# Performance work log

Measured on AMD Instinct MI355X. Metric: run time of the kernel, lower is better.

## Reference

```python
import jax, jax.numpy as jnp
import numpy as np

NUM_SLOTS, SLOT_DIM, INPUT_DIM = 4, 32, 8
NUM_ITERS = 3
SCALE = SLOT_DIM ** -0.5
LN_EPS = 1e-5


def setup_inputs() -> dict:
    key = jax.random.key(0)
    ks = jax.random.split(key, 12)
    B = 65536
    return {
        "latent": jax.random.normal(ks[0], (B, INPUT_DIM, 4, 4), jnp.float32),
        "slot_mu": jax.random.normal(ks[1], (1, NUM_SLOTS, SLOT_DIM), jnp.float32) * 0.1,
        "w_in": jax.random.normal(ks[2], (SLOT_DIM, INPUT_DIM), jnp.float32) * (INPUT_DIM ** -0.5),
        "b_in": jnp.zeros((SLOT_DIM,), jnp.float32),
        "ln_g": jnp.ones((SLOT_DIM,), jnp.float32),
        "ln_b": jnp.zeros((SLOT_DIM,), jnp.float32),
        "wq": jax.random.normal(ks[3], (SLOT_DIM, SLOT_DIM), jnp.float32) * (SLOT_DIM ** -0.5),
        "wk": jax.random.normal(ks[4], (SLOT_DIM, SLOT_DIM), jnp.float32) * (SLOT_DIM ** -0.5),
        "wv": jax.random.normal(ks[5], (SLOT_DIM, SLOT_DIM), jnp.float32) * (SLOT_DIM ** -0.5),
        "gru_wih": jax.random.normal(ks[6], (3 * SLOT_DIM, SLOT_DIM), jnp.float32) * (SLOT_DIM ** -0.5),
        "gru_whh": jax.random.normal(ks[7], (3 * SLOT_DIM, SLOT_DIM), jnp.float32) * (SLOT_DIM ** -0.5),
        "gru_bih": jnp.zeros((3 * SLOT_DIM,), jnp.float32),
        "gru_bhh": jnp.zeros((3 * SLOT_DIM,), jnp.float32),
    }


def _gru_cell(x, h, wih, whh, bih, bbh):
    # torch.nn.GRUCell math. x, h: [M, D]; weights: [3D, D]
    gi = x @ wih.T + bih  # [M, 3D]
    gh = h @ whh.T + bbh
    i_r, i_z, i_n = jnp.split(gi, 3, axis=-1)
    h_r, h_z, h_n = jnp.split(gh, 3, axis=-1)
    r = jax.nn.sigmoid(i_r + h_r)
    z = jax.nn.sigmoid(i_z + h_z)
    n = jnp.tanh(i_n + r * h_n)
    return (1.0 - z) * n + z * h


def reference(latent, slot_mu, w_in, b_in, ln_g, ln_b, wq, wk, wv,
              gru_wih, gru_whh, gru_bih, gru_bhh):
    B, C, H, W = latent.shape
    N = H * W
    x = latent.reshape(B, C, N).transpose(0, 2, 1)  # [B, N, C]
    x = x @ w_in.T + b_in                           # [B, N, D]
    mu = jnp.mean(x, axis=-1, keepdims=True)
    var = jnp.mean(jnp.square(x - mu), axis=-1, keepdims=True)
    x = (x - mu) / jnp.sqrt(var + LN_EPS) * ln_g + ln_b

    slots = jnp.broadcast_to(slot_mu, (B, NUM_SLOTS, SLOT_DIM))
    k = x @ wk.T  # [B, N, D]
    v = x @ wv.T
    for _ in range(NUM_ITERS):
        q = slots @ wq.T                                     # [B, K, D]
        attn = jnp.einsum('bkd,bnd->bkn', q, k) * SCALE      # [B, K, N]
        attn = jax.nn.softmax(attn, axis=1)                  # softmax over slots
        updates = jnp.einsum('bkn,bnd->bkd', attn, v)        # [B, K, D]
        slots = _gru_cell(updates.reshape(-1, SLOT_DIM),
                          slots.reshape(-1, SLOT_DIM),
                          gru_wih, gru_whh, gru_bih, gru_bhh).reshape(B, NUM_SLOTS, SLOT_DIM)
    return slots
```

## Files before the change

kernel.cpp:

```cpp
#include <hip/hip_runtime.h>

typedef short bf16x8 __attribute__((ext_vector_type(8)));
typedef float f32x4  __attribute__((ext_vector_type(4)));
typedef unsigned int u32x4 __attribute__((ext_vector_type(4)));

#define MFMA16(a,b,c) __builtin_amdgcn_mfma_f32_16x16x32_bf16(a,b,c,0,0,0)
#define SCALE_F 0.17677669529663687f
#define LOG2E   1.4426950408889634f

union FragU { u32x4 u4; unsigned int u[4]; bf16x8 f; };
struct WPair { bf16x8 h, l; };

__device__ __forceinline__ float fexp2(float x){ return __builtin_amdgcn_exp2f(x); }
__device__ __forceinline__ float frcp(float x){ return __builtin_amdgcn_rcpf(x); }

__device__ __forceinline__ unsigned short rne1(float x){
  unsigned int u = __float_as_uint(x);
  return (unsigned short)((u + 0x7fffu + ((u>>16)&1u)) >> 16);
}
__device__ __forceinline__ void split1(float x, unsigned short& h, unsigned short& l){
  h = rne1(x);
  float hf = __uint_as_float((unsigned)h<<16);
  l = rne1(x - hf);
}
__device__ __forceinline__ void trsplit(float x, unsigned short& h, unsigned short& l){
  unsigned int u = __float_as_uint(x);
  h = (unsigned short)(u>>16);
  l = rne1(x - __uint_as_float(u & 0xffff0000u));
}
__device__ __forceinline__ unsigned int pk32(float x){
  unsigned int u = __float_as_uint(x);
  unsigned int h = u & 0xffff0000u;
  float r = x - __uint_as_float(h);
  return h | (__float_as_uint(r) >> 16);
}
__device__ __forceinline__ void unpack8(const unsigned int* ur, FragU& hi, FragU& lo){
  #pragma unroll
  for (int i=0;i<4;++i){
    hi.u[i] = __builtin_amdgcn_perm(ur[2*i+1], ur[2*i], 0x07060302u);
    lo.u[i] = __builtin_amdgcn_perm(ur[2*i+1], ur[2*i], 0x05040100u);
  }
}
__device__ __forceinline__ f32x4 mfma3(bf16x8 ah, bf16x8 al, bf16x8 bh, bf16x8 bl, f32x4 c){
  c = MFMA16(ah, bh, c);
  c = MFMA16(al, bh, c);
  c = MFMA16(ah, bl, c);
  return c;
}

__device__ __forceinline__ void store_frag(unsigned int* ws, int t, int l, const float* v){
  FragU hh, ll;
  #pragma unroll
  for (int i=0;i<4;++i){
    unsigned short h0,l0,h1,l1;
    split1(v[2*i],   h0, l0);
    split1(v[2*i+1], h1, l1);
    hh.u[i] = (unsigned)h0 | ((unsigned)h1<<16);
    ll.u[i] = (unsigned)l0 | ((unsigned)l1<<16);
  }
  *(u32x4*)(ws + (size_t)(t*64+l)*8)     = hh.u4;
  *(u32x4*)(ws + (size_t)(t*64+l)*8 + 4) = ll.u4;
}
__device__ __forceinline__ WPair load_pre(const unsigned int* ws, int t, int l){
  const unsigned int* p = ws + (size_t)(t*64+l)*8;
  FragU a,b; a.u4 = *(const u32x4*)p; b.u4 = *(const u32x4*)(p+4);
  WPair r; r.h = a.f; r.l = b.f; return r;
}

__global__ __launch_bounds__(1024)
void prep_kernel(const float* __restrict__ wq,
                 const float* __restrict__ wk,
                 const float* __restrict__ wv,
                 const float* __restrict__ gwih,
                 const float* __restrict__ gwhh,
                 unsigned int* __restrict__ ws)
{
  __shared__ float pw[1024], pk2[1024], pf[1024];
  const int tid = threadIdx.x;
  pw[tid]  = wq[tid];
  pk2[tid] = wk[tid];
  __syncthreads();
  {
    int d = tid>>5, c = tid&31;
    float acc = 0.f;
    #pragma unroll
    for (int dp=0; dp<32; ++dp) acc = fmaf(pw[dp*32+d], pk2[dp*32+c], acc);
    pf[d*32+c] = acc * (SCALE_F * LOG2E);
  }
  __syncthreads();
  const int l = tid & 63, g = l>>4, m = l&15;
  float v[8];
  if (tid < 128){
    int t = tid>>6;
    #pragma unroll
    for (int j=0;j<8;++j) v[j] = pf[(t*16+m)*32 + 8*g + j];
    store_frag(ws, t, l, v);
  } else {
    int tile = 2 + ((tid-128)>>6);
    const float* src; float sc = 1.f;
    if (tile < 4)       { src = wv   + (tile-2)*16*32; }
    else if (tile < 10) { src = gwih + (tile-4)*16*32; sc = (tile>=8)  ? 2.f*LOG2E : LOG2E; }
    else                { src = gwhh + (tile-10)*16*32; sc = (tile>=14) ? 2.f*LOG2E : LOG2E; }
    #pragma unroll
    for (int j=0;j<8;++j) v[j] = src[m*32 + 8*g + j] * sc;
    store_frag(ws, tile, l, v);
  }
}

#define UOF 2048
#define ATO 4096
#define ZPGO 5120
#define VTO 8192

__global__ __launch_bounds__(64, 2)
void slotattn_mfma(const float* __restrict__ latent,
                   const float* __restrict__ slot_mu,
                   const float* __restrict__ w_in,
                   const float* __restrict__ b_in,
                   const float* __restrict__ ln_g,
                   const float* __restrict__ ln_b,
                   const float* __restrict__ gbih,
                   const float* __restrict__ gbhh,
                   const unsigned int* __restrict__ ws,
                   float* __restrict__ out)
{
  __shared__ __attribute__((aligned(16))) char sw[12288];
  const int l = threadIdx.x & 63;
  const int g = l >> 4;
  const int m = l & 15;
  const int batch0 = blockIdx.x * 4;
  const int xorm = (m & 7) << 4;

  {
    const float* latp = latent + (size_t)(batch0 + g) * 128 + m;
    float c[8];
    #pragma unroll
    for (int cc=0; cc<8; ++cc) c[cc] = latp[cc*16];
    float xr[32];
    #pragma unroll
    for (int d=0; d<32; ++d){
      float acc = b_in[d];
      #pragma unroll
      for (int cc=0; cc<8; ++cc) acc = fmaf(c[cc], w_in[d*8+cc], acc);
      xr[d] = acc;
    }
    float mu = 0.f;
    #pragma unroll
    for (int d=0; d<32; ++d) mu += xr[d];
    mu *= 0.03125f;
    float var = 0.f;
    #pragma unroll
    for (int d=0; d<32; ++d){ float t = xr[d]-mu; var = fmaf(t,t,var); }
    var *= 0.03125f;
    float rs = rsqrtf(var + 1e-5f);
    char* dst = sw + g*2048 + m*128;
    #pragma unroll
    for (int q=0; q<8; ++q){
      u32x4 pv;
      #pragma unroll
      for (int i=0;i<4;++i){
        int d = 4*q+i;
        pv[i] = pk32((xr[d]-mu)*rs*ln_g[d] + ln_b[d]);
      }
      *(u32x4*)(dst + ((q*16) ^ xorm)) = pv;
    }
  }
  asm volatile("" ::: "memory");

  FragU kqh[4], kql[4];
  {
    unsigned int xr8[4][8];
    #pragma unroll
    for (int bt=0; bt<4; ++bt){
      const char* base = sw + bt*2048 + m*128;
      *(u32x4*)&xr8[bt][0] = *(const u32x4*)(base + ((g*32)    ^ xorm));
      *(u32x4*)&xr8[bt][4] = *(const u32x4*)(base + ((g*32+16) ^ xorm));
    }
    asm volatile("" ::: "memory");
    WPair wf0 = load_pre(ws, 0, l), wf1 = load_pre(ws, 1, l);
    WPair wv0 = load_pre(ws, 2, l), wv1 = load_pre(ws, 3, l);
    #pragma unroll
    for (int bt=0; bt<4; ++bt){
      FragU xh, xl; unpack8(xr8[bt], xh, xl);
      f32x4 z = {0,0,0,0};
      f32x4 k0 = mfma3(xh.f, xl.f, wf0.h, wf0.l, z);
      f32x4 k1 = mfma3(xh.f, xl.f, wf1.h, wf1.l, z);
      f32x4 v0 = mfma3(xh.f, xl.f, wv0.h, wv0.l, z);
      f32x4 v1 = mfma3(xh.f, xl.f, wv1.h, wv1.l, z);
      #pragma unroll
      for (int r=0; r<4; ++r){
        int row = 4*g + r;
        int xr_ = (row & 7) << 4;
        char* kb = sw + bt*2048 + row*128;
        *(unsigned int*)(kb + ((4*m)      ^ xr_)) = pk32(k0[r]);
        *(unsigned int*)(kb + ((4*(m+16)) ^ xr_)) = pk32(k1[r]);
      }
      ushort4 pv0, pv1;
      pv0.x=rne1(v0[0]); pv0.y=rne1(v0[1]); pv0.z=rne1(v0[2]); pv0.w=rne1(v0[3]);
      pv1.x=rne1(v1[0]); pv1.y=rne1(v1[1]); pv1.z=rne1(v1[2]); pv1.w=rne1(v1[3]);
      *(ushort4*)(sw + VTO + m*128      + ((bt*32 + 8*g) ^ xorm)) = pv0;
      *(ushort4*)(sw + VTO + (m+16)*128 + ((bt*32 + 8*g) ^ xorm)) = pv1;
    }
    asm volatile("" ::: "memory");
    #pragma unroll
    for (int bt=0; bt<4; ++bt){
      const char* base = sw + bt*2048 + m*128;
      unsigned int kr[8];
      *(u32x4*)&kr[0] = *(const u32x4*)(base + ((g*32)    ^ xorm));
      *(u32x4*)&kr[4] = *(const u32x4*)(base + ((g*32+16) ^ xorm));
      unpack8(kr, kqh[bt], kql[bt]);
    }
  }
  asm volatile("" ::: "memory");

  if (l < 2){ u32x4 z = {0,0,0,0}; *(u32x4*)(sw + ZPGO + l*16) = z; }
  float hreg[8];
  #pragma unroll
  for (int T=0; T<2; ++T){
    #pragma unroll
    for (int r=0; r<4; ++r){
      float v = slot_mu[r*32 + m + 16*T];
      hreg[4*T+r] = v;
      int row = 4*g + r;
      *(unsigned int*)(sw + row*128 + ((4*(m+16*T)) ^ ((row&7)<<4))) = pk32(v);
    }
  }

  WPair wihf[6], whhf[6];
  float bihl[6], bhhl[6];
  #pragma unroll
  for (int t=0; t<6; ++t){
    wihf[t] = load_pre(ws, 4+t, l);
    whhf[t] = load_pre(ws, 10+t, l);
    float bsc = (t < 4) ? LOG2E : 2.f*LOG2E;
    bihl[t] = gbih[t*16 + m] * bsc;
    bhhl[t] = gbhh[t*16 + m] * bsc;
  }

  for (int it=0; it<3; ++it){
    asm volatile("" ::: "memory");
    unsigned int sr[8];
    {
      const char* sb = sw + m*128;
      *(u32x4*)&sr[0] = *(const u32x4*)(sb + ((g*32)    ^ xorm));
      *(u32x4*)&sr[4] = *(const u32x4*)(sb + ((g*32+16) ^ xorm));
    }
    FragU sh, sl; unpack8(sr, sh, sl);

    f32x4 ls = {0,0,0,0};
    #pragma unroll
    for (int bt=0; bt<4; ++bt){
      f32x4 z = {0,0,0,0};
      f32x4 la = mfma3(sh.f, sl.f, kqh[bt].f, kql[bt].f, z);
      if (bt==0) ls = la;
      else {
        bool take = (g==bt);
        #pragma unroll
        for (int c2=0;c2<4;++c2) ls[c2] = take ? la[c2] : ls[c2];
      }
    }
    {
      float mx = fmaxf(fmaxf(ls[0],ls[1]), fmaxf(ls[2],ls[3]));
      float e0=fexp2(ls[0]-mx), e1=fexp2(ls[1]-mx), e2=fexp2(ls[2]-mx), e3=fexp2(ls[3]-mx);
      float inv = frcp(e0+e1+e2+e3);
      float ev[4] = { e0*inv, e1*inv, e2*inv, e3*inv };
      #pragma unroll
      for (int s=0; s<4; ++s){
        unsigned short h, lo;
        trsplit(ev[s], h, lo);
        *(unsigned short*)(sw + ATO       + g*128 + s*32 + 2*m) = h;
        *(unsigned short*)(sw + ATO + 512 + g*128 + s*32 + 2*m) = lo;
      }
    }
    asm volatile("" ::: "memory");

    FragU abh[2], abl[2];
    #pragma unroll
    for (int inst=0; inst<2; ++inst){
      int bk = inst*2 + (g>>1);
      bool match = ((m>>2) == bk);
      int aoff = (m>>2)*128 + (m&3)*32 + (g&1)*16;
      abh[inst].u4 = *(const u32x4*)(match ? (sw + ATO       + aoff) : (sw + ZPGO));
      abl[inst].u4 = *(const u32x4*)(match ? (sw + ATO + 512 + aoff) : (sw + ZPGO));
    }
    f32x4 uT[2];
    #pragma unroll
    for (int T=0; T<2; ++T){
      f32x4 acc = {0,0,0,0};
      #pragma unroll
      for (int inst=0; inst<2; ++inst){
        int bk = inst*2 + (g>>1);
        FragU va;
        va.u4 = *(const u32x4*)(sw + VTO + (16*T+m)*128 + ((bk*32 + (g&1)*16) ^ xorm));
        acc = MFMA16(va.f, abh[inst].f, acc);
        acc = MFMA16(va.f, abl[inst].f, acc);
      }
      uT[T] = acc;
    }
    #pragma unroll
    for (int T=0; T<2; ++T){
      u32x4 up;
      #pragma unroll
      for (int r=0;r<4;++r) up[r] = pk32(uT[T][r]);
      *(u32x4*)(sw + UOF + m*128 + ((64*T + 16*g) ^ xorm)) = up;
    }
    asm volatile("" ::: "memory");

    unsigned int ur2[8];
    {
      const char* ub = sw + UOF + m*128;
      *(u32x4*)&ur2[0] = *(const u32x4*)(ub + ((g*32)    ^ xorm));
      *(u32x4*)&ur2[4] = *(const u32x4*)(ub + ((g*32+16) ^ xorm));
    }
    FragU uh, ul; unpack8(ur2, uh, ul);

    bool last = (it==2);
    #pragma unroll
    for (int T=0; T<2; ++T){
      f32x4 gi3[3], gh3[3];
      #pragma unroll
      for (int s3=0; s3<3; ++s3){
        int t = 2*s3 + T;
        f32x4 ci = { bihl[t], bihl[t], bihl[t], bihl[t] };
        gi3[s3] = mfma3(uh.f, ul.f, wihf[t].h, wihf[t].l, ci);
        f32x4 ch = { bhhl[t], bhhl[t], bhhl[t], bhhl[t] };
        gh3[s3] = mfma3(sh.f, sl.f, whhf[t].h, whhf[t].l, ch);
      }
      #pragma unroll
      for (int r=0; r<4; ++r){
        float rr = frcp(1.f + fexp2(-(gi3[0][r] + gh3[0][r])));
        float zz = frcp(1.f + fexp2(-(gi3[1][r] + gh3[1][r])));
        float pre = fmaf(rr, gh3[2][r], gi3[2][r]);
        float nn = fmaf(-2.f, frcp(fexp2(pre) + 1.f), 1.f);
        int d = m + 16*T;
        float hval = hreg[4*T+r];
        float hnew = fmaf(zz, hval - nn, nn);
        hreg[4*T+r] = hnew;
        if (last){
          out[(size_t)(batch0+g)*128 + r*32 + d] = hnew;
        } else {
          int row = 4*g + r;
          *(unsigned int*)(sw + row*128 + ((4*d) ^ ((row&7)<<4))) = pk32(hnew);
        }
      }
    }
  }
}

extern "C" void kernel_launch(void* const* d_in, const int* in_sizes, int n_in,
                              void* d_out, int out_size, void* d_ws, size_t ws_size,
                              hipStream_t stream) {
  const float* latent  = (const float*)d_in[0];
  const float* slot_mu = (const float*)d_in[1];
  const float* w_in    = (const float*)d_in[2];
  const float* b_in    = (const float*)d_in[3];
  const float* ln_g    = (const float*)d_in[4];
  const float* ln_b    = (const float*)d_in[5];
  const float* wq      = (const float*)d_in[6];
  const float* wk      = (const float*)d_in[7];
  const float* wv      = (const float*)d_in[8];
  const float* gwih    = (const float*)d_in[9];
  const float* gwhh    = (const float*)d_in[10];
  const float* gbih    = (const float*)d_in[11];
  const float* gbhh    = (const float*)d_in[12];
  float* out = (float*)d_out;
  unsigned int* ws = (unsigned int*)d_ws;

  prep_kernel<<<1, 1024, 0, stream>>>(wq, wk, wv, gwih, gwhh, ws);

  const int B = in_sizes[0] >> 7;
  const int grid = B >> 2;
  slotattn_mfma<<<grid, 64, 0, stream>>>(latent, slot_mu, w_in, b_in, ln_g, ln_b,
                                         gbih, gbhh, ws, out);
}
```

Measured before the change: 90.89 us.

## Process two 4-batch groups per wave and drop k low-part split

Each 64-thread block now handles 8 batch elements in two independent shared-memory stages, which halves the grid and reuses the weight fragments loaded into registers across both stages. It also stores k as plain bf16 instead of a hi/lo split, cutting the attention-logit MFMAs from three to two per tile. The cost is more registers and double the LDS per block, which may lower occupancy, and slightly reduced precision for k.

```diff
diff --git a/kernel.cpp b/kernel.cpp
--- a/kernel.cpp
+++ b/kernel.cpp
@@ -46,6 +46,12 @@
   c = MFMA16(al, bh, c);
   c = MFMA16(ah, bl, c);
   return c;
+}
+__device__ __forceinline__ bf16x8 ldfrag(const char* p){
+  FragU f;
+  *(uint2*)&f.u[0] = *(const uint2*)p;
+  *(uint2*)&f.u[2] = *(const uint2*)(p+8);
+  return f.f;
 }
 
 __device__ __forceinline__ void store_frag(unsigned int* ws, int t, int l, const float* v){
@@ -111,6 +117,7 @@
 #define ATO 4096
 #define ZPGO 5120
 #define VTO 8192
+#define SST 12288
 
 __global__ __launch_bounds__(64, 2)
 void slotattn_mfma(const float* __restrict__ latent,
@@ -124,15 +131,17 @@
                    const unsigned int* __restrict__ ws,
                    float* __restrict__ out)
 {
-  __shared__ __attribute__((aligned(16))) char sw[12288];
+  __shared__ __attribute__((aligned(16))) char smem[24576];
   const int l = threadIdx.x & 63;
   const int g = l >> 4;
   const int m = l & 15;
-  const int batch0 = blockIdx.x * 4;
+  const int batch0 = blockIdx.x * 8;
   const int xorm = (m & 7) << 4;
 
-  {
-    const float* latp = latent + (size_t)(batch0 + g) * 128 + m;
+  #pragma unroll
+  for (int st=0; st<2; ++st){
+    char* sw = smem + st*SST;
+    const float* latp = latent + (size_t)(batch0 + st*4 + g) * 128 + m;
     float c[8];
     #pragma unroll
     for (int cc=0; cc<8; ++cc) c[cc] = latp[cc*16];
@@ -167,62 +176,67 @@
   }
   asm volatile("" ::: "memory");
 
-  FragU kqh[4], kql[4];
   {
-    unsigned int xr8[4][8];
-    #pragma unroll
-    for (int bt=0; bt<4; ++bt){
-      const char* base = sw + bt*2048 + m*128;
-      *(u32x4*)&xr8[bt][0] = *(const u32x4*)(base + ((g*32)    ^ xorm));
-      *(u32x4*)&xr8[bt][4] = *(const u32x4*)(base + ((g*32+16) ^ xorm));
-    }
-    asm volatile("" ::: "memory");
     WPair wf0 = load_pre(ws, 0, l), wf1 = load_pre(ws, 1, l);
     WPair wv0 = load_pre(ws, 2, l), wv1 = load_pre(ws, 3, l);
     #pragma unroll
-    for (int bt=0; bt<4; ++bt){
-      FragU xh, xl; unpack8(xr8[bt], xh, xl);
-      f32x4 z = {0,0,0,0};
-      f32x4 k0 = mfma3(xh.f, xl.f, wf0.h, wf0.l, z);
-      f32x4 k1 = mfma3(xh.f, xl.f, wf1.h, wf1.l, z);
-      f32x4 v0 = mfma3(xh.f, xl.f, wv0.h, wv0.l, z);
-      f32x4 v1 = mfma3(xh.f, xl.f, wv1.h, wv1.l, z);
+    for (int st=0; st<2; ++st){
+      char* sw = smem + st*SST;
+      unsigned int xr8[4][8];
+      #pragma unroll
+      for (int bt=0; bt<4; ++bt){
+        const char* base = sw + bt*2048 + m*128;
+        *(u32x4*)&xr8[bt][0] = *(const u32x4*)(base + ((g*32)    ^ xorm));
+        *(u32x4*)&xr8[bt][4] = *(const u32x4*)(base + ((g*32+16) ^ xorm));
+      }
+      asm volatile("" ::: "memory");
+      #pragma unroll
+      for (int bt=0; bt<4; ++bt){
+        FragU xh, xl; unpack8(xr8[bt], xh, xl);
+        f32x4 z = {0,0,0,0};
+        f32x4 k0 = mfma3(xh.f, xl.f, wf0.h, wf0.l, z);
+        f32x4 k1 = mfma3(xh.f, xl.f, wf1.h, wf1.l, z);
+        f32x4 v0 = mfma3(xh.f, xl.f, wv0.h, wv0.l, z);
+        f32x4 v1 = mfma3(xh.f, xl.f, wv1.h, wv1.l, z);
+        #pragma unroll
+        for (int r=0; r<4; ++r){
+          int tok = 4*g + r;
+          *(unsigned short*)(sw + bt*1024 + tok*64 + 2*m)      = rne1(k0[r]);
+          *(unsigned short*)(sw + bt*1024 + tok*64 + 2*(m+16)) = rne1(k1[r]);
+        }
+        ushort4 pv0, pv1;
+        pv0.x=rne1(v0[0]); pv0.y=rne1(v0[1]); pv0.z=rne1(v0[2]); pv0.w=rne1(v0[3]);
+        pv1.x=rne1(v1[0]); pv1.y=rne1(v1[1]); pv1.z=rne1(v1[2]); pv1.w=rne1(v1[3]);
+        *(ushort4*)(sw + VTO + m*128      + ((bt*32 + 8*g) ^ xorm)) = pv0;
+        *(ushort4*)(sw + VTO + (m+16)*128 + ((bt*32 + 8*g) ^ xorm)) = pv1;
+      }
+    }
+  }
+  asm volatile("" ::: "memory");
+
+  bf16x8 kqf[2][4];
+  #pragma unroll
+  for (int st=0; st<2; ++st){
+    #pragma unroll
+    for (int bt=0; bt<4; ++bt)
+      kqf[st][bt] = ldfrag(smem + st*SST + bt*1024 + m*64 + 16*g);
+  }
+  asm volatile("" ::: "memory");
+
+  float hreg[2][8];
+  #pragma unroll
+  for (int st=0; st<2; ++st){
+    char* sw = smem + st*SST;
+    if (l < 2){ u32x4 z = {0,0,0,0}; *(u32x4*)(sw + ZPGO + l*16) = z; }
+    #pragma unroll
+    for (int T=0; T<2; ++T){
       #pragma unroll
       for (int r=0; r<4; ++r){
+        float v = slot_mu[r*32 + m + 16*T];
+        hreg[st][4*T+r] = v;
         int row = 4*g + r;
-        int xr_ = (row & 7) << 4;
-        char* kb = sw + bt*2048 + row*128;
-        *(unsigned int*)(kb + ((4*m)      ^ xr_)) = pk32(k0[r]);
-        *(unsigned int*)(kb + ((4*(m+16)) ^ xr_)) = pk32(k1[r]);
-      }
-      ushort4 pv0, pv1;
-      pv0.x=rne1(v0[0]); pv0.y=rne1(v0[1]); pv0.z=rne1(v0[2]); pv0.w=rne1(v0[3]);
-      pv1.x=rne1(v1[0]); pv1.y=rne1(v1[1]); pv1.z=rne1(v1[2]); pv1.w=rne1(v1[3]);
-      *(ushort4*)(sw + VTO + m*128      + ((bt*32 + 8*g) ^ xorm)) = pv0;
-      *(ushort4*)(sw + VTO + (m+16)*128 + ((bt*32 + 8*g) ^ xorm)) = pv1;
-    }
-    asm volatile("" ::: "memory");
-    #pragma unroll
-    for (int bt=0; bt<4; ++bt){
-      const char* base = sw + bt*2048 + m*128;
-      unsigned int kr[8];
-      *(u32x4*)&kr[0] = *(const u32x4*)(base + ((g*32)    ^ xorm));
-      *(u32x4*)&kr[4] = *(const u32x4*)(base + ((g*32+16) ^ xorm));
-      unpack8(kr, kqh[bt], kql[bt]);
-    }
-  }
-  asm volatile("" ::: "memory");
-
-  if (l < 2){ u32x4 z = {0,0,0,0}; *(u32x4*)(sw + ZPGO + l*16) = z; }
-  float hreg[8];
-  #pragma unroll
-  for (int T=0; T<2; ++T){
-    #pragma unroll
-    for (int r=0; r<4; ++r){
-      float v = slot_mu[r*32 + m + 16*T];
-      hreg[4*T+r] = v;
-      int row = 4*g + r;
-      *(unsigned int*)(sw + row*128 + ((4*(m+16*T)) ^ ((row&7)<<4))) = pk32(v);
+        *(unsigned int*)(sw + row*128 + ((4*(m+16*T)) ^ ((row&7)<<4))) = pk32(v);
+      }
     }
   }
 
@@ -239,27 +253,32 @@
 
   for (int it=0; it<3; ++it){
     asm volatile("" ::: "memory");
-    unsigned int sr[8];
-    {
-      const char* sb = sw + m*128;
+    FragU sh[2], sl[2];
+    #pragma unroll
+    for (int st=0; st<2; ++st){
+      const char* sb = smem + st*SST + m*128;
+      unsigned int sr[8];
       *(u32x4*)&sr[0] = *(const u32x4*)(sb + ((g*32)    ^ xorm));
       *(u32x4*)&sr[4] = *(const u32x4*)(sb + ((g*32+16) ^ xorm));
-    }
-    FragU sh, sl; unpack8(sr, sh, sl);
-
-    f32x4 ls = {0,0,0,0};
-    #pragma unroll
-    for (int bt=0; bt<4; ++bt){
-      f32x4 z = {0,0,0,0};
-      f32x4 la = mfma3(sh.f, sl.f, kqh[bt].f, kql[bt].f, z);
-      if (bt==0) ls = la;
-      else {
-        bool take = (g==bt);
-        #pragma unroll
-        for (int c2=0;c2<4;++c2) ls[c2] = take ? la[c2] : ls[c2];
-      }
-    }
-    {
+      unpack8(sr, sh[st], sl[st]);
+    }
+
+    #pragma unroll
+    for (int st=0; st<2; ++st){
+      char* sw = smem + st*SST;
+      f32x4 ls = {0,0,0,0};
+      #pragma unroll
+      for (int bt=0; bt<4; ++bt){
+        f32x4 z = {0,0,0,0};
+        f32x4 la = MFMA16(sh[st].f, kqf[st][bt], z);
+        la = MFMA16(sl[st].f, kqf[st][bt], la);
+        if (bt==0) ls = la;
+        else {
+          bool take = (g==bt);
+          #pragma unroll
+          for (int c2=0;c2<4;++c2) ls[c2] = take ? la[c2] : ls[c2];
+        }
+      }
       float mx = fmaxf(fmaxf(ls[0],ls[1]), fmaxf(ls[2],ls[3]));
       float e0=fexp2(ls[0]-mx), e1=fexp2(ls[1]-mx), e2=fexp2(ls[2]-mx), e3=fexp2(ls[3]-mx);
       float inv = frcp(e0+e1+e2+e3);
@@ -274,73 +293,83 @@
     }
     asm volatile("" ::: "memory");
 
-    FragU abh[2], abl[2];
-    #pragma unroll
-    for (int inst=0; inst<2; ++inst){
-      int bk = inst*2 + (g>>1);
-      bool match = ((m>>2) == bk);
-      int aoff = (m>>2)*128 + (m&3)*32 + (g&1)*16;
-      abh[inst].u4 = *(const u32x4*)(match ? (sw + ATO       + aoff) : (sw + ZPGO));
-      abl[inst].u4 = *(const u32x4*)(match ? (sw + ATO + 512 + aoff) : (sw + ZPGO));
-    }
-    f32x4 uT[2];
-    #pragma unroll
-    for (int T=0; T<2; ++T){
-      f32x4 acc = {0,0,0,0};
+    #pragma unroll
+    for (int st=0; st<2; ++st){
+      char* sw = smem + st*SST;
+      FragU abh[2], abl[2];
       #pragma unroll
       for (int inst=0; inst<2; ++inst){
         int bk = inst*2 + (g>>1);
-        FragU va;
-        va.u4 = *(const u32x4*)(sw + VTO + (16*T+m)*128 + ((bk*32 + (g&1)*16) ^ xorm));
-        acc = MFMA16(va.f, abh[inst].f, acc);
-        acc = MFMA16(va.f, abl[inst].f, acc);
-      }
-      uT[T] = acc;
-    }
-    #pragma unroll
-    for (int T=0; T<2; ++T){
-      u32x4 up;
-      #pragma unroll
-      for (int r=0;r<4;++r) up[r] = pk32(uT[T][r]);
-      *(u32x4*)(sw + UOF + m*128 + ((64*T + 16*g) ^ xorm)) = up;
+        bool match = ((m>>2) == bk);
+        int aoff = (m>>2)*128 + (m&3)*32 + (g&1)*16;
+        abh[inst].u4 = *(const u32x4*)(match ? (sw + ATO       + aoff) : (sw + ZPGO));
+        abl[inst].u4 = *(const u32x4*)(match ? (sw + ATO + 512 + aoff) : (sw + ZPGO));
+      }
+      f32x4 uT[2];
+      #pragma unroll
+      for (int T=0; T<2; ++T){
+        f32x4 acc = {0,0,0,0};
+        #pragma unroll
+        for (int inst=0; inst<2; ++inst){
+          int bk = inst*2 + (g>>1);
+          FragU va;
+          va.u4 = *(const u32x4*)(sw + VTO + (16*T+m)*128 + ((bk*32 + (g&1)*16) ^ xorm));
+          acc = MFMA16(va.f, abh[inst].f, acc);
+          acc = MFMA16(va.f, abl[inst].f, acc);
+        }
+        uT[T] = acc;
+      }
+      #pragma unroll
+      for (int T=0; T<2; ++T){
+        u32x4 up;
+        #pragma unroll
+        for (int r=0;r<4;++r) up[r] = pk32(uT[T][r]);
+        *(u32x4*)(sw + UOF + m*128 + ((64*T + 16*g) ^ xorm)) = up;
+      }
     }
     asm volatile("" ::: "memory");
 
-    unsigned int ur2[8];
-    {
-      const char* ub = sw + UOF + m*128;
+    FragU uh[2], ul[2];
+    #pragma unroll
+    for (int st=0; st<2; ++st){
+      const char* ub = smem + st*SST + UOF + m*128;
+      unsigned int ur2[8];
       *(u32x4*)&ur2[0] = *(const u32x4*)(ub + ((g*32)    ^ xorm));
       *(u32x4*)&ur2[4] = *(const u32x4*)(ub + ((g*32+16) ^ xorm));
-    }
-    FragU uh, ul; unpack8(ur2, uh, ul);
+      unpack8(ur2, uh[st], ul[st]);
+    }
 
     bool last = (it==2);
     #pragma unroll
-    for (int T=0; T<2; ++T){
-      f32x4 gi3[3], gh3[3];
-      #pragma unroll
-      for (int s3=0; s3<3; ++s3){
-        int t = 2*s3 + T;
-        f32x4 ci = { bihl[t], bihl[t], bihl[t], bihl[t] };
-        gi3[s3] = mfma3(uh.f, ul.f, wihf[t].h, wihf[t].l, ci);
-        f32x4 ch = { bhhl[t], bhhl[t], bhhl[t], bhhl[t] };
-        gh3[s3] = mfma3(sh.f, sl.f, whhf[t].h, whhf[t].l, ch);
-      }
-      #pragma unroll
-      for (int r=0; r<4; ++r){
-        float rr = frcp(1.f + fexp2(-(gi3[0][r] + gh3[0][r])));
-        float zz = frcp(1.f + fexp2(-(gi3[1][r] + gh3[1][r])));
-        float pre = fmaf(rr, gh3[2][r], gi3[2][r]);
-        float nn = fmaf(-2.f, frcp(fexp2(pre) + 1.f), 1.f);
-        int d = m + 16*T;
-        float hval = hreg[4*T+r];
-        float hnew = fmaf(zz, hval - nn, nn);
-        hreg[4*T+r] = hnew;
-        if (last){
-          out[(size_t)(batch0+g)*128 + r*32 + d] = hnew;
-        } else {
-          int row = 4*g + r;
-          *(unsigned int*)(sw + row*128 + ((4*d) ^ ((row&7)<<4))) = pk32(hnew);
+    for (int st=0; st<2; ++st){
+      char* sw = smem + st*SST;
+      #pragma unroll
+      for (int T=0; T<2; ++T){
+        f32x4 gi3[3], gh3[3];
+        #pragma unroll
+        for (int s3=0; s3<3; ++s3){
+          int t = 2*s3 + T;
+          f32x4 ci = { bihl[t], bihl[t], bihl[t], bihl[t] };
+          gi3[s3] = mfma3(uh[st].f, ul[st].f, wihf[t].h, wihf[t].l, ci);
+          f32x4 ch = { bhhl[t], bhhl[t], bhhl[t], bhhl[t] };
+          gh3[s3] = mfma3(sh[st].f, sl[st].f, whhf[t].h, whhf[t].l, ch);
+        }
+        #pragma unroll
+        for (int r=0; r<4; ++r){
+          float rr = frcp(1.f + fexp2(-(gi3[0][r] + gh3[0][r])));
+          float zz = frcp(1.f + fexp2(-(gi3[1][r] + gh3[1][r])));
+          float pre = fmaf(rr, gh3[2][r], gi3[2][r]);
+          float nn = fmaf(-2.f, frcp(fexp2(pre) + 1.f), 1.f);
+          int d = m + 16*T;
+          float hval = hreg[st][4*T+r];
+          float hnew = fmaf(zz, hval - nn, nn);
+          hreg[st][4*T+r] = hnew;
+          if (last){
+            out[(size_t)(batch0 + st*4 + g)*128 + r*32 + d] = hnew;
+          } else {
+            int row = 4*g + r;
+            *(unsigned int*)(sw + row*128 + ((4*d) ^ ((row&7)<<4))) = pk32(hnew);
+          }
         }
       }
     }
@@ -369,7 +398,7 @@
   prep_kernel<<<1, 1024, 0, stream>>>(wq, wk, wv, gwih, gwhh, ws);
 
   const int B = in_sizes[0] >> 7;
-  const int grid = B >> 2;
+  const int grid = B >> 3;
   slotattn_mfma<<<grid, 64, 0, stream>>>(latent, slot_mu, w_in, b_in, ln_g, ln_b,
                                          gbih, gbhh, ws, out);
 }
```

After: 192.3 us. 2.12x slower.
